# Optimization experiments

Hardware: AMD Instinct MI355X
Metric: run time of the kernel (lower is better)

## Reference

```python
import jax, jax.numpy as jnp
import numpy as np

B, S, D, H, DFF = 2, 2048, 1024, 16, 4096
DK = D // H
EPS = 1e-6


def layer_norm(x, alpha, bias):
    # TF reduce_std is biased std; eps added to std (not variance)
    mean = jnp.mean(x, axis=-1, keepdims=True)
    std = jnp.sqrt(jnp.mean((x - mean) ** 2, axis=-1, keepdims=True))
    return alpha * (x - mean) / (std + EPS) + bias


def setup_inputs() -> dict:
    key = jax.random.key(0)
    ks = jax.random.split(key, 10)
    s = 0.02
    return {
        "x": jax.random.normal(ks[0], (B, S, D), jnp.float32),
        "mask": jnp.ones((B, 1, 1, S), jnp.int32),
        "wq": jax.random.normal(ks[1], (D, D), jnp.float32) * s,
        "wk": jax.random.normal(ks[2], (D, D), jnp.float32) * s,
        "wv": jax.random.normal(ks[3], (D, D), jnp.float32) * s,
        "wo": jax.random.normal(ks[4], (D, D), jnp.float32) * s,
        "w1": jax.random.normal(ks[5], (D, DFF), jnp.float32) * s,
        "b1": jnp.zeros((DFF,), jnp.float32),
        "w2": jax.random.normal(ks[6], (DFF, D), jnp.float32) * s,
        "b2": jnp.zeros((D,), jnp.float32),
        "ln1_a": jnp.ones((D,), jnp.float32),
        "ln1_b": jnp.zeros((D,), jnp.float32),
        "ln2_a": jnp.ones((D,), jnp.float32),
        "ln2_b": jnp.zeros((D,), jnp.float32),
    }


def reference(x, mask, wq, wk, wv, wo, w1, b1, w2, b2, ln1_a, ln1_b, ln2_a, ln2_b):
    # --- residual 1: pre-norm self-attention ---
    xn = layer_norm(x, ln1_a, ln1_b)
    q = (xn @ wq).reshape(B, S, H, DK)
    k = (xn @ wk).reshape(B, S, H, DK)
    v = (xn @ wv).reshape(B, S, H, DK)
    scores = jnp.einsum('bqhd,bkhd->bhqk', q, k) / jnp.sqrt(jnp.float32(DK))
    scores = jnp.where(mask == 0, jnp.float32(-1e9), scores)
    attn = jax.nn.softmax(scores, axis=-1)  # dropout = identity at eval
    ctx = jnp.einsum('bhqk,bkhd->bqhd', attn, v).reshape(B, S, D)
    x = x + ctx @ wo
    # --- residual 2: pre-norm FFN ---
    xn = layer_norm(x, ln2_a, ln2_b)
    ff = jax.nn.relu(xn @ w1 + b1) @ w2 + b2
    return x + ff
```

## Files before the change

kernel.cpp:

```cpp
#include <hip/hip_runtime.h>

#define BATCH 2
#define SEQ   2048
#define DMODEL 1024
#define NHEAD 16
#define DHEAD 64
#define DFF_  4096
#define MROWS (BATCH*SEQ)
#define EPS 1e-6f

typedef unsigned short u16;
typedef unsigned int u32;
typedef __bf16 bf16x8 __attribute__((ext_vector_type(8)));
typedef float  f32x4  __attribute__((ext_vector_type(4)));
typedef u32    u32x2  __attribute__((ext_vector_type(2)));

__device__ __forceinline__ float bf2f(u16 h) {
    union { u32 u; float f; } v; v.u = ((u32)h) << 16; return v.f;
}
__device__ __forceinline__ u16 f2bf(float f) {
    union { float f; u32 u; } v; v.f = f;
    u32 u = v.u;
    u32 r = (u + 0x7fffu + ((u >> 16) & 1u)) >> 16;
    return (u16)r;
}

__device__ __forceinline__ void async16(const u16* g, u16* l) {
    __builtin_amdgcn_global_load_lds((const __attribute__((address_space(1))) void*)g,
                                     (__attribute__((address_space(3))) void*)l,
                                     16, 0, 0);
}

__global__ __launch_bounds__(256) void transpose_cvt(const float* __restrict__ in,
                                                     u16* __restrict__ out,
                                                     int R, int C) {
    __shared__ float tile[32][33];
    int c0 = blockIdx.x * 32, r0 = blockIdx.y * 32;
    int x = threadIdx.x, y = threadIdx.y;
    #pragma unroll
    for (int i = 0; i < 32; i += 8)
        tile[y + i][x] = in[(size_t)(r0 + y + i) * C + c0 + x];
    __syncthreads();
    #pragma unroll
    for (int i = 0; i < 32; i += 8)
        out[(size_t)(c0 + y + i) * R + r0 + x] = f2bf(tile[x][y + i]);
}

__global__ __launch_bounds__(256) void transpose_v_perm(const u16* __restrict__ qkv,
                                                        u16* __restrict__ vtp) {
    __shared__ u16 tile[64][72];
    int kt = blockIdx.x * 64;
    int bh = blockIdx.y; int b = bh >> 4, h = bh & 15;
    const u16* in = qkv + ((size_t)(b * SEQ + kt)) * 3072 + 2 * DMODEL + h * DHEAD;
    u16* out = vtp + ((size_t)bh * DHEAD) * SEQ;
    int t = threadIdx.x;
    int r = t >> 3, c8 = (t & 7) * 8;
    #pragma unroll
    for (int pass = 0; pass < 2; pass++) {
        int row = r + pass * 32;
        uint4 v = *(const uint4*)(in + (size_t)row * 3072 + c8);
        *(uint4*)&tile[row][c8] = v;
    }
    __syncthreads();
    #pragma unroll
    for (int pass = 0; pass < 2; pass++) {
        int d = r + pass * 32;
        u16 o8[8];
        #pragma unroll
        for (int e = 0; e < 8; e++) {
            int c = c8 + e;
            o8[e] = tile[(c & 3) * 16 + (c >> 2)][d];
        }
        *(uint4*)(out + (size_t)d * SEQ + kt + c8) = *(const uint4*)o8;
    }
}

__global__ __launch_bounds__(256) void ln_kernel(const float* __restrict__ x,
                                                 const float* __restrict__ alpha,
                                                 const float* __restrict__ beta,
                                                 u16* __restrict__ out) {
    int row = blockIdx.x;
    int t = threadIdx.x;
    const float* xr = x + (size_t)row * DMODEL;
    float4 xv = ((const float4*)xr)[t];
    float f0 = xv.x, f1 = xv.y, f2 = xv.z, f3 = xv.w;
    float s1 = f0 + f1 + f2 + f3;
    float s2 = f0*f0 + f1*f1 + f2*f2 + f3*f3;
    #pragma unroll
    for (int off = 32; off >= 1; off >>= 1) {
        s1 += __shfl_xor(s1, off);
        s2 += __shfl_xor(s2, off);
    }
    __shared__ float r1[4], r2[4];
    int w = t >> 6, lane = t & 63;
    if (lane == 0) { r1[w] = s1; r2[w] = s2; }
    __syncthreads();
    s1 = r1[0] + r1[1] + r1[2] + r1[3];
    s2 = r2[0] + r2[1] + r2[2] + r2[3];
    float mean = s1 * (1.0f / DMODEL);
    float var  = s2 * (1.0f / DMODEL) - mean * mean;
    var = fmaxf(var, 0.0f);
    float inv = 1.0f / (sqrtf(var) + EPS);
    float4 av = ((const float4*)alpha)[t];
    float4 bv = ((const float4*)beta)[t];
    ushort4 ov;
    ov.x = f2bf(av.x * (f0 - mean) * inv + bv.x);
    ov.y = f2bf(av.y * (f1 - mean) * inv + bv.y);
    ov.z = f2bf(av.z * (f2 - mean) * inv + bv.z);
    ov.w = f2bf(av.w * (f3 - mean) * inv + bv.w);
    ((ushort4*)(out + (size_t)row * DMODEL))[t] = ov;
}

#define BK 64

template <int AI, int AJ, bool OUT_F32>
__global__ __launch_bounds__(256) void gemm_bt(const u16* __restrict__ A,
                                               const u16* __restrict__ BT,
                                               void* __restrict__ Cp,
                                               const float* __restrict__ bias,
                                               const float* __restrict__ residual,
                                               int M, int N, int K, int do_relu) {
    constexpr int BMt = AI * 32, BNt = AJ * 32;
    __shared__ u16 As[BMt * BK];
    __shared__ u16 Bs[BNt * BK];
    int t = threadIdx.x;
    int m0 = blockIdx.y * BMt, n0 = blockIdx.x * BNt;
    int lane = t & 63, w = t >> 6;
    int wr = w >> 1, wc = w & 1;
    int lhi = lane >> 4, llo = lane & 15;
    int sr = lane >> 3, sk = lane & 7;
    int skx = (sk ^ sr) * 8;

    f32x4 acc[AI][AJ] = {};

    const u16* Ab = A  + (size_t)m0 * K + skx;
    const u16* Bb = BT + (size_t)n0 * K + skx;

    for (int k0 = 0; k0 < K; k0 += BK) {
        __syncthreads();
        #pragma unroll
        for (int j = 0; j < AI; j++) {
            int blk = w * AI + j;
            async16(Ab + (size_t)(blk * 8 + sr) * K + k0, &As[blk * 512]);
        }
        #pragma unroll
        for (int j = 0; j < AJ; j++) {
            int blk = w * AJ + j;
            async16(Bb + (size_t)(blk * 8 + sr) * K + k0, &Bs[blk * 512]);
        }
        __syncthreads();
        #pragma unroll
        for (int kk = 0; kk < 2; kk++) {
            int slot = ((kk * 4 + lhi) ^ (llo & 7)) * 8;
            bf16x8 af[AI], bfr[AJ];
            #pragma unroll
            for (int i = 0; i < AI; i++)
                af[i]  = *(const bf16x8*)(&As[(wr * 16 * AI + i * 16 + llo) * 64 + slot]);
            #pragma unroll
            for (int j = 0; j < AJ; j++)
                bfr[j] = *(const bf16x8*)(&Bs[(wc * 16 * AJ + j * 16 + llo) * 64 + slot]);
            #pragma unroll
            for (int i = 0; i < AI; i++)
                #pragma unroll
                for (int j = 0; j < AJ; j++)
                    acc[i][j] = __builtin_amdgcn_mfma_f32_16x16x32_bf16(af[i], bfr[j], acc[i][j], 0, 0, 0);
        }
    }

    #pragma unroll
    for (int i = 0; i < AI; i++) {
        #pragma unroll
        for (int rr = 0; rr < 4; rr++) {
            int row = m0 + wr * 16 * AI + i * 16 + lhi * 4 + rr;
            #pragma unroll
            for (int j = 0; j < AJ; j++) {
                int col = n0 + wc * 16 * AJ + j * 16 + llo;
                float v = acc[i][j][rr];
                if (bias)      v += bias[col];
                if (residual)  v += residual[(size_t)row * N + col];
                if (do_relu)   v = fmaxf(v, 0.0f);
                size_t idx = (size_t)row * N + col;
                if (OUT_F32) ((float*)Cp)[idx] = v;
                else         ((u16*)Cp)[idx]   = f2bf(v);
            }
        }
    }
}

#define PSTR 72
#define SCL 0.18033688f

__global__ __launch_bounds__(128) void flash_attn(const u16* __restrict__ qkv,
                                                  const u16* __restrict__ vtp,
                                                  const int* __restrict__ mask,
                                                  u16* __restrict__ ctx) {
    __shared__ u16 QPs[2 * 32 * PSTR];
    __shared__ u16 Ks[64 * 64];
    __shared__ u16 VTs[64 * 64];
    __shared__ float mbias[64];

    int t = threadIdx.x;
    int wv = t >> 6, lane = t & 63, lhi = lane >> 4, llo = lane & 15;
    int sr = lane >> 3, sk = lane & 7;
    int skx = (sk ^ sr) * 8;
    int q0 = blockIdx.x * 64, h = blockIdx.y, b = blockIdx.z;

    const u16* Qg  = qkv + ((size_t)(b * SEQ + q0)) * 3072 + h * DHEAD;
    const u16* Kg  = qkv + ((size_t)(b * SEQ)) * 3072 + DMODEL + h * DHEAD;
    const u16* VTg = vtp + ((size_t)((b * NHEAD + h) * DHEAD)) * SEQ;

    #pragma unroll
    for (int j = 0; j < 4; j++) {
        int blk = wv * 4 + j;
        async16(Qg + (size_t)(blk * 8 + sr) * 3072 + skx, &QPs[blk * 512]);
    }
    __syncthreads();
    bf16x8 qf[2][2];
    #pragma unroll
    for (int mi = 0; mi < 2; mi++)
        #pragma unroll
        for (int kk = 0; kk < 2; kk++)
            qf[mi][kk] = *(const bf16x8*)&QPs[(wv * 32 + mi * 16 + llo) * 64 +
                                              ((kk * 4 + lhi) ^ (llo & 7)) * 8];

    u16* Ps = QPs + wv * (32 * PSTR);

    float l_part[2][4] = {};
    f32x4 o_acc[2][4] = {};

    for (int kt = 0; kt < SEQ; kt += 64) {
        __syncthreads();
        #pragma unroll
        for (int j = 0; j < 4; j++) {
            int blk = wv * 4 + j;
            async16(Kg  + (size_t)(kt + blk * 8 + sr) * 3072 + skx, &Ks[blk * 512]);
            async16(VTg + (size_t)(blk * 8 + sr) * SEQ + kt + skx,  &VTs[blk * 512]);
        }
        if (t < 64) mbias[t] = (mask[b * SEQ + kt + t] == 0) ? -1.0e12f : 0.0f;
        __syncthreads();

        f32x4 s0[4] = {}, s1[4] = {};
        #pragma unroll
        for (int kk = 0; kk < 2; kk++) {
            #pragma unroll
            for (int j = 0; j < 4; j++) {
                bf16x8 kf = *(const bf16x8*)&Ks[(j * 16 + llo) * 64 +
                                                ((kk * 4 + lhi) ^ (llo & 7)) * 8];
                s0[j] = __builtin_amdgcn_mfma_f32_16x16x32_bf16(qf[0][kk], kf, s0[j], 0, 0, 0);
                s1[j] = __builtin_amdgcn_mfma_f32_16x16x32_bf16(qf[1][kk], kf, s1[j], 0, 0, 0);
            }
        }
        float mb[4];
        #pragma unroll
        for (int j = 0; j < 4; j++) mb[j] = mbias[j * 16 + llo];

        #pragma unroll
        for (int mi = 0; mi < 2; mi++) {
            const f32x4* s = mi ? s1 : s0;
            #pragma unroll
            for (int rr = 0; rr < 4; rr++) {
                u32 pu[4];
                #pragma unroll
                for (int j = 0; j < 4; j++) {
                    float p = __builtin_amdgcn_exp2f(__builtin_fmaf(s[j][rr], SCL, mb[j]));
                    l_part[mi][rr] += p;
                    union { float f; u32 u; } c; c.f = p;
                    pu[j] = c.u;
                }
                u32x2 w;
                w[0] = (pu[0] >> 16) | (pu[1] & 0xffff0000u);
                w[1] = (pu[2] >> 16) | (pu[3] & 0xffff0000u);
                *(u32x2*)&Ps[(mi * 16 + lhi * 4 + rr) * PSTR + llo * 4] = w;
            }
        }
        #pragma unroll
        for (int kk = 0; kk < 2; kk++) {
            bf16x8 pf0 = *(const bf16x8*)&Ps[(0 * 16 + llo) * PSTR + kk * 32 + lhi * 8];
            bf16x8 pf1 = *(const bf16x8*)&Ps[(1 * 16 + llo) * PSTR + kk * 32 + lhi * 8];
            #pragma unroll
            for (int nb = 0; nb < 4; nb++) {
                bf16x8 vf = *(const bf16x8*)&VTs[(nb * 16 + llo) * 64 +
                                                 ((kk * 4 + lhi) ^ (llo & 7)) * 8];
                o_acc[0][nb] = __builtin_amdgcn_mfma_f32_16x16x32_bf16(pf0, vf, o_acc[0][nb], 0, 0, 0);
                o_acc[1][nb] = __builtin_amdgcn_mfma_f32_16x16x32_bf16(pf1, vf, o_acc[1][nb], 0, 0, 0);
            }
        }
    }

    #pragma unroll
    for (int mi = 0; mi < 2; mi++) {
        #pragma unroll
        for (int rr = 0; rr < 4; rr++) {
            float l = l_part[mi][rr];
            #pragma unroll
            for (int off = 1; off <= 8; off <<= 1) l += __shfl_xor(l, off);
            float inv = __builtin_amdgcn_rcpf(l);
            int row = q0 + wv * 32 + mi * 16 + lhi * 4 + rr;
            #pragma unroll
            for (int nb = 0; nb < 4; nb++) {
                int col = h * DHEAD + nb * 16 + llo;
                ctx[((size_t)(b * SEQ) + row) * DMODEL + col] = f2bf(o_acc[mi][nb][rr] * inv);
            }
        }
    }
}

extern "C" void kernel_launch(void* const* d_in, const int* in_sizes, int n_in,
                              void* d_out, int out_size, void* d_ws, size_t ws_size,
                              hipStream_t stream) {
    (void)in_sizes; (void)n_in; (void)out_size; (void)ws_size;
    const float* x    = (const float*)d_in[0];
    const int* mask   = (const int*)d_in[1];
    const float* wq   = (const float*)d_in[2];
    const float* wk   = (const float*)d_in[3];
    const float* wv   = (const float*)d_in[4];
    const float* wo   = (const float*)d_in[5];
    const float* w1   = (const float*)d_in[6];
    const float* b1   = (const float*)d_in[7];
    const float* w2   = (const float*)d_in[8];
    const float* b2   = (const float*)d_in[9];
    const float* ln1a = (const float*)d_in[10];
    const float* ln1b = (const float*)d_in[11];
    const float* ln2a = (const float*)d_in[12];
    const float* ln2b = (const float*)d_in[13];
    float* out = (float*)d_out;

    char* wsb = (char*)d_ws;
    const size_t MB = 1024 * 1024;
    u16*   wqkvT = (u16*)(wsb + 0);
    u16*   woT   = (u16*)(wsb + 6 * MB);
    u16*   w1T   = (u16*)(wsb + 8 * MB);
    u16*   w2T   = (u16*)(wsb + 16 * MB);
    u16*   xn    = (u16*)(wsb + 24 * MB);
    float* x2    = (float*)(wsb + 32 * MB);
    u16*   vtp   = (u16*)(wsb + 32 * MB);
    u16*   ctx   = (u16*)(wsb + 48 * MB);
    u16*   qkv   = (u16*)(wsb + 56 * MB);
    u16*   ff1   = (u16*)(wsb + 56 * MB);

    dim3 tb(32, 8);
    transpose_cvt<<<dim3(DMODEL/32, DMODEL/32), tb, 0, stream>>>(wq, wqkvT,               DMODEL, DMODEL);
    transpose_cvt<<<dim3(DMODEL/32, DMODEL/32), tb, 0, stream>>>(wk, wqkvT + 1024*1024,   DMODEL, DMODEL);
    transpose_cvt<<<dim3(DMODEL/32, DMODEL/32), tb, 0, stream>>>(wv, wqkvT + 2*1024*1024, DMODEL, DMODEL);
    transpose_cvt<<<dim3(DMODEL/32, DMODEL/32), tb, 0, stream>>>(wo, woT,                 DMODEL, DMODEL);
    transpose_cvt<<<dim3(DFF_/32,  DMODEL/32),  tb, 0, stream>>>(w1, w1T,                 DMODEL, DFF_);
    transpose_cvt<<<dim3(DMODEL/32, DFF_/32),   tb, 0, stream>>>(w2, w2T,                 DFF_, DMODEL);

    ln_kernel<<<MROWS, 256, 0, stream>>>(x, ln1a, ln1b, xn);
    gemm_bt<4,4,false><<<dim3(3072/128, MROWS/128), 256, 0, stream>>>(xn, wqkvT, qkv,
                                                                      nullptr, nullptr,
                                                                      MROWS, 3072, DMODEL, 0);
    transpose_v_perm<<<dim3(SEQ/64, BATCH*NHEAD), 256, 0, stream>>>(qkv, vtp);
    flash_attn<<<dim3(SEQ/64, NHEAD, BATCH), 128, 0, stream>>>(qkv, vtp, mask, ctx);
    gemm_bt<2,2,true><<<dim3(DMODEL/64, MROWS/64), 256, 0, stream>>>(ctx, woT, x2,
                                                                     nullptr, x,
                                                                     MROWS, DMODEL, DMODEL, 0);
    ln_kernel<<<MROWS, 256, 0, stream>>>(x2, ln2a, ln2b, xn);
    gemm_bt<4,4,false><<<dim3(DFF_/128, MROWS/128), 256, 0, stream>>>(xn, w1T, ff1,
                                                                     b1, nullptr,
                                                                     MROWS, DFF_, DMODEL, 1);
    gemm_bt<2,2,true><<<dim3(DMODEL/64, MROWS/64), 256, 0, stream>>>(ff1, w2T, out,
                                                                    b2, x2,
                                                                    MROWS, DMODEL, DFF_, 0);
}
```

Before: 401.1 us.

## Split flash attention Q tile across four waves with swizzled P buffer

The attention block now runs 256 threads (four waves) per 64-query tile, with each wave owning 16 query rows instead of two waves owning 32 rows each. The padded P staging buffer is replaced by an XOR-swizzled 64-wide layout that reuses the Q shared buffer, so LDS stays the same. The aim is more waves per block for latency hiding and fewer registers per thread. In exchange, each K/V tile loaded to LDS is reused by fewer MFMAs per wave, and four waves now share every barrier.

```diff
diff --git a/kernel.cpp b/kernel.cpp
--- a/kernel.cpp
+++ b/kernel.cpp
@@ -187,20 +187,19 @@
     }
 }
 
-#define PSTR 72
 #define SCL 0.18033688f
 
-__global__ __launch_bounds__(128) void flash_attn(const u16* __restrict__ qkv,
+__global__ __launch_bounds__(256) void flash_attn(const u16* __restrict__ qkv,
                                                   const u16* __restrict__ vtp,
                                                   const int* __restrict__ mask,
                                                   u16* __restrict__ ctx) {
-    __shared__ u16 QPs[2 * 32 * PSTR];
+    __shared__ u16 QPs[64 * 64];
     __shared__ u16 Ks[64 * 64];
     __shared__ u16 VTs[64 * 64];
     __shared__ float mbias[64];
 
     int t = threadIdx.x;
-    int wv = t >> 6, lane = t & 63, lhi = lane >> 4, llo = lane & 15;
+    int w = t >> 6, lane = t & 63, lhi = lane >> 4, llo = lane & 15;
     int sr = lane >> 3, sk = lane & 7;
     int skx = (sk ^ sr) * 8;
     int q0 = blockIdx.x * 64, h = blockIdx.y, b = blockIdx.z;
@@ -210,44 +209,40 @@
     const u16* VTg = vtp + ((size_t)((b * NHEAD + h) * DHEAD)) * SEQ;
 
     #pragma unroll
-    for (int j = 0; j < 4; j++) {
-        int blk = wv * 4 + j;
+    for (int j = 0; j < 2; j++) {
+        int blk = w * 2 + j;
         async16(Qg + (size_t)(blk * 8 + sr) * 3072 + skx, &QPs[blk * 512]);
     }
     __syncthreads();
-    bf16x8 qf[2][2];
-    #pragma unroll
-    for (int mi = 0; mi < 2; mi++)
-        #pragma unroll
-        for (int kk = 0; kk < 2; kk++)
-            qf[mi][kk] = *(const bf16x8*)&QPs[(wv * 32 + mi * 16 + llo) * 64 +
-                                              ((kk * 4 + lhi) ^ (llo & 7)) * 8];
-
-    u16* Ps = QPs + wv * (32 * PSTR);
-
-    float l_part[2][4] = {};
-    f32x4 o_acc[2][4] = {};
+    bf16x8 qf[2];
+    #pragma unroll
+    for (int kk = 0; kk < 2; kk++)
+        qf[kk] = *(const bf16x8*)&QPs[(w * 16 + llo) * 64 + ((kk * 4 + lhi) ^ (llo & 7)) * 8];
+
+    u16* Ps = QPs + w * 1024;
+
+    float l_part[4] = {};
+    f32x4 o_acc[4] = {};
 
     for (int kt = 0; kt < SEQ; kt += 64) {
         __syncthreads();
         #pragma unroll
-        for (int j = 0; j < 4; j++) {
-            int blk = wv * 4 + j;
+        for (int j = 0; j < 2; j++) {
+            int blk = w * 2 + j;
             async16(Kg  + (size_t)(kt + blk * 8 + sr) * 3072 + skx, &Ks[blk * 512]);
             async16(VTg + (size_t)(blk * 8 + sr) * SEQ + kt + skx,  &VTs[blk * 512]);
         }
         if (t < 64) mbias[t] = (mask[b * SEQ + kt + t] == 0) ? -1.0e12f : 0.0f;
         __syncthreads();
 
-        f32x4 s0[4] = {}, s1[4] = {};
+        f32x4 s[4] = {};
         #pragma unroll
         for (int kk = 0; kk < 2; kk++) {
             #pragma unroll
             for (int j = 0; j < 4; j++) {
                 bf16x8 kf = *(const bf16x8*)&Ks[(j * 16 + llo) * 64 +
                                                 ((kk * 4 + lhi) ^ (llo & 7)) * 8];
-                s0[j] = __builtin_amdgcn_mfma_f32_16x16x32_bf16(qf[0][kk], kf, s0[j], 0, 0, 0);
-                s1[j] = __builtin_amdgcn_mfma_f32_16x16x32_bf16(qf[1][kk], kf, s1[j], 0, 0, 0);
+                s[j] = __builtin_amdgcn_mfma_f32_16x16x32_bf16(qf[kk], kf, s[j], 0, 0, 0);
             }
         }
         float mb[4];
@@ -255,52 +250,44 @@
         for (int j = 0; j < 4; j++) mb[j] = mbias[j * 16 + llo];
 
         #pragma unroll
-        for (int mi = 0; mi < 2; mi++) {
-            const f32x4* s = mi ? s1 : s0;
-            #pragma unroll
-            for (int rr = 0; rr < 4; rr++) {
-                u32 pu[4];
-                #pragma unroll
-                for (int j = 0; j < 4; j++) {
-                    float p = __builtin_amdgcn_exp2f(__builtin_fmaf(s[j][rr], SCL, mb[j]));
-                    l_part[mi][rr] += p;
-                    union { float f; u32 u; } c; c.f = p;
-                    pu[j] = c.u;
-                }
-                u32x2 w;
-                w[0] = (pu[0] >> 16) | (pu[1] & 0xffff0000u);
-                w[1] = (pu[2] >> 16) | (pu[3] & 0xffff0000u);
-                *(u32x2*)&Ps[(mi * 16 + lhi * 4 + rr) * PSTR + llo * 4] = w;
+        for (int rr = 0; rr < 4; rr++) {
+            u32 pu[4];
+            #pragma unroll
+            for (int j = 0; j < 4; j++) {
+                float p = __builtin_amdgcn_exp2f(__builtin_fmaf(s[j][rr], SCL, mb[j]));
+                l_part[rr] += p;
+                union { float f; u32 u; } c; c.f = p;
+                pu[j] = c.u;
             }
+            u32x2 pw;
+            pw[0] = (pu[0] >> 16) | (pu[1] & 0xffff0000u);
+            pw[1] = (pu[2] >> 16) | (pu[3] & 0xffff0000u);
+            int prow = lhi * 4 + rr;
+            *(u32x2*)&Ps[prow * 64 + ((llo >> 1) ^ (prow & 7)) * 8 + (llo & 1) * 4] = pw;
         }
         #pragma unroll
         for (int kk = 0; kk < 2; kk++) {
-            bf16x8 pf0 = *(const bf16x8*)&Ps[(0 * 16 + llo) * PSTR + kk * 32 + lhi * 8];
-            bf16x8 pf1 = *(const bf16x8*)&Ps[(1 * 16 + llo) * PSTR + kk * 32 + lhi * 8];
+            bf16x8 pf = *(const bf16x8*)&Ps[llo * 64 + ((kk * 4 + lhi) ^ (llo & 7)) * 8];
             #pragma unroll
             for (int nb = 0; nb < 4; nb++) {
                 bf16x8 vf = *(const bf16x8*)&VTs[(nb * 16 + llo) * 64 +
                                                  ((kk * 4 + lhi) ^ (llo & 7)) * 8];
-                o_acc[0][nb] = __builtin_amdgcn_mfma_f32_16x16x32_bf16(pf0, vf, o_acc[0][nb], 0, 0, 0);
-                o_acc[1][nb] = __builtin_amdgcn_mfma_f32_16x16x32_bf16(pf1, vf, o_acc[1][nb], 0, 0, 0);
+                o_acc[nb] = __builtin_amdgcn_mfma_f32_16x16x32_bf16(pf, vf, o_acc[nb], 0, 0, 0);
             }
         }
     }
 
     #pragma unroll
-    for (int mi = 0; mi < 2; mi++) {
-        #pragma unroll
-        for (int rr = 0; rr < 4; rr++) {
-            float l = l_part[mi][rr];
-            #pragma unroll
-            for (int off = 1; off <= 8; off <<= 1) l += __shfl_xor(l, off);
-            float inv = __builtin_amdgcn_rcpf(l);
-            int row = q0 + wv * 32 + mi * 16 + lhi * 4 + rr;
-            #pragma unroll
-            for (int nb = 0; nb < 4; nb++) {
-                int col = h * DHEAD + nb * 16 + llo;
-                ctx[((size_t)(b * SEQ) + row) * DMODEL + col] = f2bf(o_acc[mi][nb][rr] * inv);
-            }
+    for (int rr = 0; rr < 4; rr++) {
+        float l = l_part[rr];
+        #pragma unroll
+        for (int off = 1; off <= 8; off <<= 1) l += __shfl_xor(l, off);
+        float inv = __builtin_amdgcn_rcpf(l);
+        int row = q0 + w * 16 + lhi * 4 + rr;
+        #pragma unroll
+        for (int nb = 0; nb < 4; nb++) {
+            int col = h * DHEAD + nb * 16 + llo;
+            ctx[((size_t)(b * SEQ) + row) * DMODEL + col] = f2bf(o_acc[nb][rr] * inv);
         }
     }
 }
@@ -351,7 +338,7 @@
                                                                       nullptr, nullptr,
                                                                       MROWS, 3072, DMODEL, 0);
     transpose_v_perm<<<dim3(SEQ/64, BATCH*NHEAD), 256, 0, stream>>>(qkv, vtp);
-    flash_attn<<<dim3(SEQ/64, NHEAD, BATCH), 128, 0, stream>>>(qkv, vtp, mask, ctx);
+    flash_attn<<<dim3(SEQ/64, NHEAD, BATCH), 256, 0, stream>>>(qkv, vtp, mask, ctx);
     gemm_bt<2,2,true><<<dim3(DMODEL/64, MROWS/64), 256, 0, stream>>>(ctx, woT, x2,
                                                                      nullptr, x,
                                                                      MROWS, DMODEL, DMODEL, 0);
```

Result: faster. 386.9 us (-3.5%).
